# Kernel optimization log

Measured on AMD Instinct MI355X. Metric: run time of the kernel, lower is better.

The kernel has to match this reference:

```python
import jax, jax.numpy as jnp
import numpy as np

C = 1024
H = C // 64          # 16 heads
CH = 64              # head dim
NUM_BUCKETS = 32
MAX_DISTANCE = 64
REL_SCALE = float(np.sqrt(CH))  # (channels//num_heads)**0.5 = 8
EPS = 1e-5


def group_norm(x, gamma, beta, groups):
    # x: [B, C, T]
    B, Cc, T = x.shape
    xg = x.reshape(B, groups, -1)
    m = xg.mean(-1, keepdims=True)
    v = xg.var(-1, keepdims=True)
    xn = ((xg - m) * jax.lax.rsqrt(v + EPS)).reshape(B, Cc, T)
    return xn * gamma[None, :, None] + beta[None, :, None]


def conv1d(x, w, b, pad):
    # x: [B, Cin, T], w: [Cout, Cin, K]
    y = jax.lax.conv_general_dilated(x, w, (1,), [(pad, pad)],
                                     dimension_numbers=('NCH', 'OIH', 'NCH'))
    return y + b[None, :, None]


def rel_pos_bias(T, emb):
    # lucidrains RelativePositionBias, non-causal; emb: [num_buckets, H]
    pos = jnp.arange(T)
    n = pos[:, None] - pos[None, :]          # n = -(k - q) = q - k
    half = NUM_BUCKETS // 2                  # 16
    ret = (n < 0).astype(jnp.int32) * half
    n = jnp.abs(n)
    max_exact = half // 2                    # 8
    is_small = n < max_exact
    nf = jnp.maximum(n, 1).astype(jnp.float32)
    val_large = max_exact + (jnp.log(nf / max_exact)
                             / np.log(MAX_DISTANCE / max_exact)
                             * (half - max_exact)).astype(jnp.int32)
    val_large = jnp.minimum(val_large, half - 1)
    bucket = ret + jnp.where(is_small, n, val_large)  # [T, T]
    return emb[bucket].transpose(2, 0, 1)             # [H, T, T]


def setup_inputs() -> dict:
    key = jax.random.key(0)
    ks = jax.random.split(key, 20)
    B, T = 8, 1024
    s = 0.02
    return {
        'x': jax.random.normal(ks[0], (B, C, T), jnp.float32),
        # ResBlock in_layers
        'rb_gn1_g': jnp.ones((C,), jnp.float32),
        'rb_gn1_b': jnp.zeros((C,), jnp.float32),
        'rb_conv1_w': jax.random.normal(ks[1], (C, C, 3), jnp.float32) * s,
        'rb_conv1_b': jnp.zeros((C,), jnp.float32),
        # ResBlock out_layers (zero-init in original; randomized for testing)
        'rb_gn2_g': jnp.ones((C,), jnp.float32),
        'rb_gn2_b': jnp.zeros((C,), jnp.float32),
        'rb_conv2_w': jax.random.normal(ks[2], (C, C, 3), jnp.float32) * s,
        'rb_conv2_b': jnp.zeros((C,), jnp.float32),
        # outer GroupNorm(8, C)
        'norm_g': jnp.ones((C,), jnp.float32),
        'norm_b': jnp.zeros((C,), jnp.float32),
        # AttentionBlock
        'attn_gn_g': jnp.ones((C,), jnp.float32),
        'attn_gn_b': jnp.zeros((C,), jnp.float32),
        'qkv_w': jax.random.normal(ks[3], (3 * C, C, 1), jnp.float32) * s,
        'qkv_b': jnp.zeros((3 * C,), jnp.float32),
        'proj_w': jax.random.normal(ks[4], (C, C, 1), jnp.float32) * s,
        'proj_b': jnp.zeros((C,), jnp.float32),
        'rel_emb': jax.random.normal(ks[5], (NUM_BUCKETS, H), jnp.float32) * s,
    }


def reference(x, rb_gn1_g, rb_gn1_b, rb_conv1_w, rb_conv1_b,
              rb_gn2_g, rb_gn2_b, rb_conv2_w, rb_conv2_b,
              norm_g, norm_b, attn_gn_g, attn_gn_b,
              qkv_w, qkv_b, proj_w, proj_b, rel_emb):
    B, Cc, T = x.shape
    # ResBlock: GN32 -> SiLU -> conv3 -> GN32 -> SiLU -> (dropout=0) -> conv3, + skip
    h = jax.nn.silu(group_norm(x, rb_gn1_g, rb_gn1_b, 32))
    h = conv1d(h, rb_conv1_w, rb_conv1_b, 1)
    h = jax.nn.silu(group_norm(h, rb_gn2_g, rb_gn2_b, 32))
    h = conv1d(h, rb_conv2_w, rb_conv2_b, 1)
    h = x + h
    # outer GroupNorm(8)
    h = group_norm(h, norm_g, norm_b, 8)
    # AttentionBlock with relative position bias
    xin = h
    qkv = conv1d(group_norm(h, attn_gn_g, attn_gn_b, 32), qkv_w, qkv_b, 0)
    # channel layout after reshape(bs*H, 3*ch, T): [H, 3, ch]
    qkv = qkv.reshape(B, H, 3, CH, T)
    q, k, v = qkv[:, :, 0], qkv[:, :, 1], qkv[:, :, 2]
    scale = CH ** -0.25
    w = jnp.einsum('bhct,bhcs->bhts', q * scale, k * scale)
    bias = rel_pos_bias(T, rel_emb) * REL_SCALE       # [H, T, T]
    w = jax.nn.softmax((w + bias[None]).astype(jnp.float32), axis=-1).astype(w.dtype)
    a = jnp.einsum('bhts,bhcs->bhct', w, v).reshape(B, Cc, T)
    return xin + conv1d(a, proj_w, proj_b, 0)
```

## Files before the change

### kernel.cpp

```cpp
#include <hip/hip_runtime.h>

typedef __attribute__((ext_vector_type(4))) float f32x4;
typedef __attribute__((ext_vector_type(8))) __bf16 bf16x8;
typedef __attribute__((ext_vector_type(4))) unsigned short us4;
typedef __attribute__((ext_vector_type(8))) unsigned short us8;

#define DEVI static __device__ __forceinline__

DEVI unsigned short f2bf(float f){
  union { float f; unsigned u; } x; x.f = f;
  unsigned r = x.u + 0x7fffu + ((x.u >> 16) & 1u);
  return (unsigned short)(r >> 16);
}
DEVI float bf2f(unsigned short h){
  union { unsigned u; float f; } x; x.u = ((unsigned)h) << 16;
  return x.f;
}

typedef __attribute__((address_space(1))) unsigned int gu32;
typedef __attribute__((address_space(3))) unsigned int lu32;
DEVI void gll16(const void* g, void* l){
  __builtin_amdgcn_global_load_lds((gu32*)g, (lu32*)l, 16, 0, 0);
}

DEVI f32x4 mfma16(bf16x8 a, bf16x8 b, f32x4 c){
  return __builtin_amdgcn_mfma_f32_16x16x32_bf16(a, b, c, 0, 0, 0);
}

DEVI float wredsum(float v){
  #pragma unroll
  for (int m = 1; m < 64; m <<= 1) v += __shfl_xor(v, m);
  return v;
}

__global__ __launch_bounds__(256) void conv_w_prep(const float* __restrict__ w,
                                                   unsigned short* __restrict__ wp){
  int idx = blockIdx.x * 256 + threadIdx.x;
  const float* p = w + (size_t)idx * 3;
  wp[idx]           = f2bf(p[0]);
  wp[1048576 + idx] = f2bf(p[1]);
  wp[2097152 + idx] = f2bf(p[2]);
}

__global__ __launch_bounds__(256) void cast_f2b(const float* __restrict__ in,
                                                unsigned short* __restrict__ out, int n4){
  int idx = blockIdx.x * 256 + threadIdx.x;
  if (idx < n4){
    f32x4 v = *(const f32x4*)&in[(size_t)idx * 4];
    us4 o;
    #pragma unroll
    for (int j = 0; j < 4; j++) o[j] = f2bf(v[j]);
    *(us4*)&out[(size_t)idx * 4] = o;
  }
}

__global__ __launch_bounds__(256) void btab_k(const float* __restrict__ emb,
                                              float* __restrict__ btab){
  int idx = blockIdx.x * 256 + threadIdx.x;
  if (idx >= 2047 * 16) return;
  int d = idx >> 4, h = idx & 15;
  int n0 = d - 1023;
  int ret = (n0 < 0) ? 16 : 0;
  int n = (n0 < 0) ? -n0 : n0;
  int bucket;
  if (n < 8) bucket = ret + n;
  else {
    float ratio = logf((float)n * 0.125f) / 2.0794415416798357f;
    int vl = 8 + (int)(ratio * 8.0f);
    bucket = ret + (vl < 15 ? vl : 15);
  }
  btab[h * 2048 + d] = emb[bucket * 16 + h] * 11.541560327111707f;
}

__global__ __launch_bounds__(256) void zero_pads(unsigned short* __restrict__ h1p,
                                                 unsigned short* __restrict__ g2p){
  int idx = blockIdx.x * 256 + threadIdx.x;
  int b = idx >> 11, rr = (idx >> 10) & 1, c = idx & 1023;
  size_t off = ((size_t)b * 1026 + (rr ? 1025 : 0)) * 1024 + c;
  h1p[off] = 0; g2p[off] = 0;
}

__global__ __launch_bounds__(256) void gn_stats_cast(const float* __restrict__ in,
                                                     float2* __restrict__ st,
                                                     unsigned short* __restrict__ xb){
  const int g = blockIdx.x; const int tid = threadIdx.x;
  const float* p = in + (size_t)g * 32768;
  unsigned short* q = xb + (size_t)g * 32768;
  float s = 0.f, s2 = 0.f;
  for (int i = tid * 4; i < 32768; i += 1024){
    f32x4 v = *(const f32x4*)&p[i];
    us4 o;
    #pragma unroll
    for (int j = 0; j < 4; j++){ s += v[j]; s2 += v[j] * v[j]; o[j] = f2bf(v[j]); }
    *(us4*)&q[i] = o;
  }
  s = wredsum(s); s2 = wredsum(s2);
  __shared__ float rs[4], rs2[4];
  if ((tid & 63) == 0){ rs[tid >> 6] = s; rs2[tid >> 6] = s2; }
  __syncthreads();
  if (tid == 0){
    float S = rs[0] + rs[1] + rs[2] + rs[3];
    float S2 = rs2[0] + rs2[1] + rs2[2] + rs2[3];
    float m = S * (1.f / 32768.f);
    float var = S2 * (1.f / 32768.f) - m * m;
    st[g] = make_float2(m, rsqrtf(var + 1e-5f));
  }
}

__global__ __launch_bounds__(256) void gn_stats_bf16(const unsigned short* __restrict__ in,
                                                     float2* __restrict__ st){
  const int g = blockIdx.x; const int tid = threadIdx.x;
  const unsigned short* p = in + (size_t)g * 32768;
  float s = 0.f, s2 = 0.f;
  for (int i = tid * 8; i < 32768; i += 2048){
    us8 v = *(const us8*)&p[i];
    #pragma unroll
    for (int j = 0; j < 8; j++){ float f = bf2f(v[j]); s += f; s2 += f * f; }
  }
  s = wredsum(s); s2 = wredsum(s2);
  __shared__ float rs[4], rs2[4];
  if ((tid & 63) == 0){ rs[tid >> 6] = s; rs2[tid >> 6] = s2; }
  __syncthreads();
  if (tid == 0){
    float S = rs[0] + rs[1] + rs[2] + rs[3];
    float S2 = rs2[0] + rs2[1] + rs2[2] + rs2[3];
    float m = S * (1.f / 32768.f);
    float var = S2 * (1.f / 32768.f) - m * m;
    st[g] = make_float2(m, rsqrtf(var + 1e-5f));
  }
}

template<int SILU, int INBF16, int OUTPAD>
__global__ __launch_bounds__(256) void gn_apply_tr(
    const void* __restrict__ inp, const float2* __restrict__ st,
    const float* __restrict__ gma, const float* __restrict__ bta,
    unsigned short* __restrict__ out)
{
  const int gid = blockIdx.x;
  const int tc = gid & 15, g = (gid >> 4) & 31, b = gid >> 9;
  const int tid = threadIdx.x;
  const int t0 = tc * 64;
  __shared__ __align__(16) unsigned short tr[64 * 40];
  float2 s = st[b * 32 + g];
  int c = tid >> 3, t8 = (tid & 7) * 8;
  int ch = g * 32 + c;
  float sc = gma[ch] * s.y;
  float sh = bta[ch] - s.x * sc;
  float vv[8];
  if (INBF16){
    const unsigned short* p = (const unsigned short*)inp + ((size_t)b * 1024 + ch) * 1024 + t0 + t8;
    us8 v = *(const us8*)p;
    #pragma unroll
    for (int j = 0; j < 8; j++) vv[j] = bf2f(v[j]);
  } else {
    const float* p = (const float*)inp + ((size_t)b * 1024 + ch) * 1024 + t0 + t8;
    f32x4 v0 = *(const f32x4*)p; f32x4 v1 = *(const f32x4*)(p + 4);
    #pragma unroll
    for (int j = 0; j < 4; j++){ vv[j] = v0[j]; vv[4 + j] = v1[j]; }
  }
  #pragma unroll
  for (int j = 0; j < 8; j++){
    float v = vv[j] * sc + sh;
    if (SILU) v = v / (1.f + __expf(-v));
    tr[(t8 + j) * 40 + c] = f2bf(v);
  }
  __syncthreads();
  int t = tid >> 2, c8 = (tid & 3) * 8;
  us8 d = *(const us8*)&tr[t * 40 + c8];
  size_t row = OUTPAD ? ((size_t)b * 1026 + 1 + t0 + t) : ((size_t)b * 1024 + t0 + t);
  *(us8*)&out[row * 1024 + g * 32 + c8] = d;
}

__global__ __launch_bounds__(256) void gn2_partial(const unsigned short* __restrict__ c1,
                                                   float2* __restrict__ part){
  const int tid = threadIdx.x;
  const int ck = blockIdx.x & 31, b = blockIdx.x >> 5;
  const unsigned short* p = c1 + ((size_t)b * 1024 + ck * 32) * 1024 + tid * 4;
  float s = 0.f, s2 = 0.f;
  for (int r = 0; r < 32; r++){
    us4 v = *(const us4*)&p[(size_t)r * 1024];
    #pragma unroll
    for (int j = 0; j < 4; j++){ float f = bf2f(v[j]); s += f; s2 += f * f; }
  }
  __shared__ float ls[256], ls2[256];
  ls[tid] = s; ls2[tid] = s2;
  __syncthreads();
  if (tid < 32){
    float S = 0.f, S2 = 0.f;
    #pragma unroll
    for (int k = 0; k < 8; k++){ S += ls[tid * 8 + k]; S2 += ls2[tid * 8 + k]; }
    part[((size_t)b * 32 + ck) * 32 + tid] = make_float2(S, S2);
  }
}

template<int SILU>
__global__ __launch_bounds__(256) void gn2_apply(const unsigned short* __restrict__ c1,
    const float2* __restrict__ part, const float* __restrict__ gma, const float* __restrict__ bta,
    unsigned short* __restrict__ outp)
{
  const int tid = threadIdx.x;
  const int ck = blockIdx.x & 31, b = blockIdx.x >> 5;
  __shared__ float2 st[32];
  if (tid < 32){
    float S = 0.f, S2 = 0.f;
    for (int k = 0; k < 32; k++){ float2 pp = part[((size_t)b * 32 + k) * 32 + tid]; S += pp.x; S2 += pp.y; }
    float m = S * (1.f / 32768.f);
    float var = S2 * (1.f / 32768.f) - m * m;
    st[tid] = make_float2(m, rsqrtf(var + 1e-5f));
  }
  __syncthreads();
  float2 s = st[tid >> 3];
  float sc[4], sh[4];
  #pragma unroll
  for (int j = 0; j < 4; j++){ int ch = tid * 4 + j; sc[j] = gma[ch] * s.y; sh[j] = bta[ch] - s.x * sc[j]; }
  const unsigned short* p = c1 + ((size_t)b * 1024 + ck * 32) * 1024 + tid * 4;
  unsigned short* q = outp + ((size_t)b * 1026 + 1 + ck * 32) * 1024 + tid * 4;
  for (int r = 0; r < 32; r++){
    us4 v = *(const us4*)&p[(size_t)r * 1024];
    us4 o;
    #pragma unroll
    for (int j = 0; j < 4; j++){
      float f = bf2f(v[j]) * sc[j] + sh[j];
      if (SILU) f = f / (1.f + __expf(-f));
      o[j] = f2bf(f);
    }
    *(us4*)&q[(size_t)r * 1024] = o;
  }
}

__global__ __launch_bounds__(256) void gn8_partial(const unsigned short* __restrict__ r,
                                                   float2* __restrict__ part){
  const int gid = blockIdx.x; const int tid = threadIdx.x;
  const int sub = gid & 15, g = (gid >> 4) & 7, b = gid >> 7;
  const unsigned short* p = r + ((size_t)(b * 8 + g)) * 131072 + sub * 8192;
  float s = 0.f, s2 = 0.f;
  for (int i = tid * 8; i < 8192; i += 2048){
    us8 v = *(const us8*)&p[i];
    #pragma unroll
    for (int j = 0; j < 8; j++){ float f = bf2f(v[j]); s += f; s2 += f * f; }
  }
  s = wredsum(s); s2 = wredsum(s2);
  __shared__ float rs[4], rs2[4];
  if ((tid & 63) == 0){ rs[tid >> 6] = s; rs2[tid >> 6] = s2; }
  __syncthreads();
  if (tid == 0) part[gid] = make_float2(rs[0] + rs[1] + rs[2] + rs[3],
                                        rs2[0] + rs2[1] + rs2[2] + rs2[3]);
}

__global__ __launch_bounds__(256) void gn8_apply(const unsigned short* __restrict__ r,
    const float2* __restrict__ part, const float* __restrict__ gma, const float* __restrict__ bta,
    unsigned short* __restrict__ xin){
  const int gid = blockIdx.x; const int tid = threadIdx.x;
  const int sub = gid & 15, g = (gid >> 4) & 7, b = gid >> 7;
  __shared__ float2 stt;
  if (tid == 0){
    float S = 0.f, S2 = 0.f;
    #pragma unroll
    for (int k = 0; k < 16; k++){ float2 pp = part[(gid & ~15) + k]; S += pp.x; S2 += pp.y; }
    float m = S * (1.f / 131072.f);
    float var = S2 * (1.f / 131072.f) - m * m;
    stt = make_float2(m, rsqrtf(var + 1e-5f));
  }
  __syncthreads();
  float2 s = stt;
  const unsigned short* pr = r + ((size_t)(b * 8 + g)) * 131072 + sub * 8192;
  unsigned short* px = xin + ((size_t)(b * 8 + g)) * 131072 + sub * 8192;
  for (int i = tid * 8; i < 8192; i += 2048){
    int c = g * 128 + sub * 8 + (i >> 10);
    float sc = gma[c] * s.y, sh = bta[c] - s.x * sc;
    us8 v = *(const us8*)&pr[i];
    us8 o;
    #pragma unroll
    for (int j = 0; j < 8; j++) o[j] = f2bf(bf2f(v[j]) * sc + sh);
    *(us8*)&px[i] = o;
  }
}

template<int KK, int EPI>
__global__ __launch_bounds__(256, 2) void gemm_k(
    const unsigned short* __restrict__ inT,
    const unsigned short* __restrict__ W,
    const float* __restrict__ bias,
    void* __restrict__ outp,
    void* __restrict__ resp,
    int OC, int NT)
{
  __shared__ __align__(16) unsigned short Alds[128 * 64];
  __shared__ __align__(16) unsigned short Blds[128 * 64];
  const int tid = threadIdx.x;
  const int lane = tid & 63;
  const int w = tid >> 6;
  const int wn = w >> 1, wo = w & 1;
  const int nt = blockIdx.x % NT;
  const int ot = blockIdx.x / NT;
  const int b = nt >> 3;
  const int t0 = (nt & 7) * 128;
  const int ob = ot * 128;
  const int rowbase = (KK == 3) ? (b * 1026 + t0) : (b * 1024 + t0);

  f32x4 acc[4][4];
  #pragma unroll
  for (int m = 0; m < 4; m++)
    #pragma unroll
    for (int n = 0; n < 4; n++) acc[m][n] = 0.f;

  const int lrow = lane >> 3;
  const int lblk = lane & 7;

  for (int kk = 0; kk < KK; ++kk){
    const unsigned short* Ab = inT + (size_t)(rowbase + kk) * 1024;
    const unsigned short* Bb = W + ((size_t)kk * OC + ob) * 1024;
    for (int i0 = 0; i0 < 1024; i0 += 64){
      #pragma unroll
      for (int j = 0; j < 4; ++j){
        int chunk = w * 4 + j;
        int row = chunk * 8 + lrow;
        int gcol = (lblk ^ (row & 7)) * 8;
        gll16(Ab + (size_t)row * 1024 + i0 + gcol, &Alds[chunk * 512]);
        gll16(Bb + (size_t)row * 1024 + i0 + gcol, &Blds[chunk * 512]);
      }
      __syncthreads();
      bf16x8 af[2][4], bfv[2][4];
      #pragma unroll
      for (int m = 0; m < 4; m++){
        int row = wn * 64 + m * 16 + (lane & 15);
        #pragma unroll
        for (int k2 = 0; k2 < 2; k2++){
          int blk = ((lane >> 4) + k2 * 4) ^ (row & 7);
          af[k2][m] = *(const bf16x8*)&Alds[row * 64 + blk * 8];
        }
      }
      #pragma unroll
      for (int n = 0; n < 4; n++){
        int row = wo * 64 + n * 16 + (lane & 15);
        #pragma unroll
        for (int k2 = 0; k2 < 2; k2++){
          int blk = ((lane >> 4) + k2 * 4) ^ (row & 7);
          bfv[k2][n] = *(const bf16x8*)&Blds[row * 64 + blk * 8];
        }
      }
      #pragma unroll
      for (int k2 = 0; k2 < 2; k2++)
        #pragma unroll
        for (int m = 0; m < 4; m++)
          #pragma unroll
          for (int n = 0; n < 4; n++)
            acc[m][n] = mfma16(af[k2][m], bfv[k2][n], acc[m][n]);
      __syncthreads();
    }
  }

  if (EPI == 0){
    unsigned short* out = (unsigned short*)outp;
    #pragma unroll
    for (int m = 0; m < 4; m++){
      int tl = t0 + wn * 64 + m * 16 + ((lane >> 4) * 4);
      #pragma unroll
      for (int n = 0; n < 4; n++){
        int o = ob + wo * 64 + n * 16 + (lane & 15);
        float bz = bias[o];
        size_t base = ((size_t)b * 1024 + tl) * OC + o;
        #pragma unroll
        for (int r = 0; r < 4; r++)
          out[base + (size_t)r * OC] = f2bf(acc[m][n][r] + bz);
      }
    }
  } else if (EPI == 3){
    unsigned short* qkT = (unsigned short*)outp;
    unsigned short* vT  = (unsigned short*)resp;
    #pragma unroll
    for (int m = 0; m < 4; m++){
      int tl = t0 + wn * 64 + m * 16 + ((lane >> 4) * 4);
      #pragma unroll
      for (int n = 0; n < 4; n++){
        int o0 = ob + wo * 64 + n * 16;
        int h = o0 / 192;
        int rem0 = o0 - h * 192;
        int o = o0 + (lane & 15);
        float bz = bias[o];
        if (rem0 < 128){
          size_t base = ((size_t)b * 1024 + tl) * 2048 + h * 128 + rem0 + (lane & 15);
          #pragma unroll
          for (int r = 0; r < 4; r++)
            qkT[base + (size_t)r * 2048] = f2bf(acc[m][n][r] + bz);
        } else {
          int c = rem0 - 128 + (lane & 15);
          size_t base = (((size_t)(b * 16 + h)) * 64 + c) * 1024 + tl;
          us4 o4;
          #pragma unroll
          for (int r = 0; r < 4; r++) o4[r] = f2bf(acc[m][n][r] + bz);
          *(us4*)&vT[base] = o4;
        }
      }
    }
  } else if (EPI == 4){
    unsigned short* out = (unsigned short*)outp;
    const unsigned short* xr = (const unsigned short*)resp;
    #pragma unroll
    for (int m = 0; m < 4; m++){
      int tl = t0 + wn * 64 + m * 16 + ((lane >> 4) * 4);
      #pragma unroll
      for (int n = 0; n < 4; n++){
        int o = ob + wo * 64 + n * 16 + (lane & 15);
        float bz = bias[o];
        size_t base = ((size_t)b * 1024 + o) * 1024 + tl;
        us4 xv = *(const us4*)&xr[base];
        us4 ov;
        #pragma unroll
        for (int r = 0; r < 4; r++) ov[r] = f2bf(bf2f(xv[r]) + acc[m][n][r] + bz);
        *(us4*)&out[base] = ov;
      }
    }
  } else {
    float* out = (float*)outp;
    #pragma unroll
    for (int m = 0; m < 4; m++){
      int tl = t0 + wn * 64 + m * 16 + ((lane >> 4) * 4);
      #pragma unroll
      for (int n = 0; n < 4; n++){
        int o = ob + wo * 64 + n * 16 + (lane & 15);
        float bz = bias[o];
        size_t base = ((size_t)b * 1024 + o) * 1024 + tl;
        const unsigned short* xr = (const unsigned short*)resp;
        us4 xv = *(const us4*)&xr[base];
        f32x4 v;
        v[0] = bf2f(xv[0]); v[1] = bf2f(xv[1]); v[2] = bf2f(xv[2]); v[3] = bf2f(xv[3]);
        #pragma unroll
        for (int r = 0; r < 4; r++) v[r] += acc[m][n][r] + bz;
        *(f32x4*)&out[base] = v;
      }
    }
  }
}

__global__ __launch_bounds__(256, 2) void attn_k5(
    const unsigned short* __restrict__ qkT,
    const unsigned short* __restrict__ vT,
    const float* __restrict__ btab,
    unsigned short* __restrict__ aT)
{
  __shared__ __align__(16) unsigned short Kb[2][64 * 64];
  __shared__ __align__(16) unsigned short Vb[2][64 * 64];
  __shared__ __align__(16) unsigned short Pb[4][32 * 64];
  __shared__ __align__(16) float blds[1152];
  const int tid = threadIdx.x, lane = tid & 63, w = tid >> 6;
  const int d0 = blockIdx.x;
  const int xcd = d0 & 7, slot = d0 >> 3;
  const int bh = xcd * 16 + (slot >> 3);
  const int qt = slot & 7;
  const int h = bh & 15, b = bh >> 4;
  const int q0b = qt * 128;
  const int q0 = q0b + w * 32;
  const unsigned short* qk = qkT + (size_t)b * 1024 * 2048 + h * 128;
  const unsigned short* vh = vT + ((size_t)(b * 16 + h)) * 64 * 1024;
  const int lc = lane & 15, lg = lane >> 4;

  const float bneg = btab[h * 2048 + 0];
  const float bpos = btab[h * 2048 + 2046];

  for (int i = tid; i < 1151; i += 256)
    blds[i] = btab[h * 2048 + q0b + i];

  bf16x8 qf[2][2];
  #pragma unroll
  for (int m = 0; m < 2; m++){
    const unsigned short* qrow = qk + (size_t)(q0 + m * 16 + lc) * 2048;
    #pragma unroll
    for (int k2 = 0; k2 < 2; k2++)
      qf[m][k2] = *(const bf16x8*)&qrow[k2 * 32 + lg * 8];
  }
  float m_run[2], l_run[2];
  f32x4 oacc[2][4];
  m_run[0] = m_run[1] = -1e30f; l_run[0] = l_run[1] = 0.f;
  #pragma unroll
  for (int m = 0; m < 2; m++)
    #pragma unroll
    for (int cb = 0; cb < 4; cb++) oacc[m][cb] = 0.f;

  const int lr = lane >> 3, lb = lane & 7;
  const float qs = 0.18033688011112042f;

  #pragma unroll
  for (int j = 0; j < 2; j++){
    int chunk = w * 2 + j;
    int row = chunk * 8 + lr;
    int gcol = (lb ^ (row & 7)) * 8;
    gll16(qk + 64 + (size_t)row * 2048 + gcol, &Kb[0][chunk * 512]);
    gll16(vh + (size_t)row * 1024 + gcol, &Vb[0][chunk * 512]);
  }
  __syncthreads();

  for (int t = 0; t < 16; ++t){
    const int cur = t & 1;
    const int st0 = t * 64;
    if (t < 15){
      int nst = st0 + 64;
      #pragma unroll
      for (int j = 0; j < 2; j++){
        int chunk = w * 2 + j;
        int row = chunk * 8 + lr;
        int gcol = (lb ^ (row & 7)) * 8;
        gll16(qk + 64 + (size_t)(nst + row) * 2048 + gcol, &Kb[cur ^ 1][chunk * 512]);
        gll16(vh + (size_t)row * 1024 + nst + gcol, &Vb[cur ^ 1][chunk * 512]);
      }
    }
    f32x4 sfr[2][4];
    #pragma unroll
    for (int m = 0; m < 2; m++)
      #pragma unroll
      for (int sub = 0; sub < 4; sub++) sfr[m][sub] = 0.f;
    __builtin_amdgcn_s_setprio(1);
    #pragma unroll
    for (int sub = 0; sub < 4; sub++){
      int row = sub * 16 + lc;
      #pragma unroll
      for (int k2 = 0; k2 < 2; k2++){
        int blk = (lg + k2 * 4) ^ (row & 7);
        bf16x8 bk = *(const bf16x8*)&Kb[cur][row * 64 + blk * 8];
        sfr[0][sub] = mfma16(bk, qf[0][k2], sfr[0][sub]);
        sfr[1][sub] = mfma16(bk, qf[1][k2], sfr[1][sub]);
      }
    }
    __builtin_amdgcn_s_setprio(0);
    const bool unineg = (st0 >= q0 + 81);
    const bool unipos = (st0 + 113 <= q0);
    const bool uni = unineg || unipos;
    const float bc = unineg ? bneg : bpos;
    float pm2[2];
    if (uni){
      #pragma unroll
      for (int m = 0; m < 2; m++){
        float x0 = fmaxf(fmaxf(sfr[m][0][0], sfr[m][0][1]), fmaxf(sfr[m][0][2], sfr[m][0][3]));
        float x1 = fmaxf(fmaxf(sfr[m][1][0], sfr[m][1][1]), fmaxf(sfr[m][1][2], sfr[m][1][3]));
        float x2 = fmaxf(fmaxf(sfr[m][2][0], sfr[m][2][1]), fmaxf(sfr[m][2][2], sfr[m][2][3]));
        float x3 = fmaxf(fmaxf(sfr[m][3][0], sfr[m][3][1]), fmaxf(sfr[m][3][2], sfr[m][3][3]));
        float pm = fmaxf(fmaxf(x0, x1), fmaxf(x2, x3)) * qs + bc;
        pm = fmaxf(pm, __shfl_xor(pm, 16));
        pm = fmaxf(pm, __shfl_xor(pm, 32));
        pm2[m] = pm;
      }
    } else {
      #pragma unroll
      for (int m = 0; m < 2; m++){
        const float* bp = &blds[(w * 32 + m * 16 + lc) + 960 - st0];
        #pragma unroll
        for (int sub = 0; sub < 4; sub++){
          int off = 63 - sub * 16 - lg * 4;
          #pragma unroll
          for (int r = 0; r < 4; r++)
            sfr[m][sub][r] = sfr[m][sub][r] * qs + bp[off - r];
        }
        float x0 = fmaxf(fmaxf(sfr[m][0][0], sfr[m][0][1]), fmaxf(sfr[m][0][2], sfr[m][0][3]));
        float x1 = fmaxf(fmaxf(sfr[m][1][0], sfr[m][1][1]), fmaxf(sfr[m][1][2], sfr[m][1][3]));
        float x2 = fmaxf(fmaxf(sfr[m][2][0], sfr[m][2][1]), fmaxf(sfr[m][2][2], sfr[m][2][3]));
        float x3 = fmaxf(fmaxf(sfr[m][3][0], sfr[m][3][1]), fmaxf(sfr[m][3][2], sfr[m][3][3]));
        float pm = fmaxf(fmaxf(x0, x1), fmaxf(x2, x3));
        pm = fmaxf(pm, __shfl_xor(pm, 16));
        pm = fmaxf(pm, __shfl_xor(pm, 32));
        pm2[m] = pm;
      }
    }
    const bool stable = (pm2[0] <= m_run[0] + 8.f) && (pm2[1] <= m_run[1] + 8.f);
    const bool resc = !__all(stable);
    float corr[2], mref[2];
    if (resc){
      #pragma unroll
      for (int m = 0; m < 2; m++){
        float mn = fmaxf(m_run[m], pm2[m]);
        corr[m] = exp2f(m_run[m] - mn);
        m_run[m] = mn; mref[m] = mn;
      }
    } else { mref[0] = m_run[0]; mref[1] = m_run[1]; }
    const float scl = uni ? qs : 1.f;
    #pragma unroll
    for (int m = 0; m < 2; m++){
      const float ad = (uni ? bc : 0.f) - mref[m];
      float ssum = 0.f;
      #pragma unroll
      for (int sub = 0; sub < 4; sub++)
        #pragma unroll
        for (int r = 0; r < 4; r++){
          float e = exp2f(fmaf(sfr[m][sub][r], scl, ad));
          sfr[m][sub][r] = e;
          ssum += e;
        }
      ssum += __shfl_xor(ssum, 16);
      ssum += __shfl_xor(ssum, 32);
      l_run[m] = resc ? (l_run[m] * corr[m] + ssum) : (l_run[m] + ssum);
    }
    if (resc){
      #pragma unroll
      for (int m = 0; m < 2; m++)
        #pragma unroll
        for (int r = 0; r < 4; r++){
          float co = __shfl(corr[m], lg * 4 + r);
          #pragma unroll
          for (int cb = 0; cb < 4; cb++) oacc[m][cb][r] *= co;
        }
    }
    unsigned short* P = &Pb[w][0];
    #pragma unroll
    for (int m = 0; m < 2; m++){
      int qrow = m * 16 + lc;
      int rsw = (qrow & 7) << 3;
      #pragma unroll
      for (int sub = 0; sub < 4; sub++){
        int col = sub * 16 + lg * 4;
        unsigned w0, w1;
        asm("v_cvt_pk_bf16_f32 %0, %1, %2" : "=v"(w0) : "v"(sfr[m][sub][0]), "v"(sfr[m][sub][1]));
        asm("v_cvt_pk_bf16_f32 %0, %1, %2" : "=v"(w1) : "v"(sfr[m][sub][2]), "v"(sfr[m][sub][3]));
        uint2 pk; pk.x = w0; pk.y = w1;
        *(uint2*)&P[qrow * 64 + (col ^ rsw)] = pk;
      }
    }
    __builtin_amdgcn_s_setprio(1);
    #pragma unroll
    for (int k2 = 0; k2 < 2; k2++){
      bf16x8 pa[2];
      #pragma unroll
      for (int m = 0; m < 2; m++){
        int rowp = m * 16 + lc;
        int blkp = (lg + k2 * 4) ^ (rowp & 7);
        pa[m] = *(const bf16x8*)&P[rowp * 64 + blkp * 8];
      }
      #pragma unroll
      for (int cb = 0; cb < 4; cb++){
        int ch = cb * 16 + lc;
        int blkv = (lg + k2 * 4) ^ (ch & 7);
        bf16x8 bv = *(const bf16x8*)&Vb[cur][ch * 64 + blkv * 8];
        oacc[0][cb] = mfma16(pa[0], bv, oacc[0][cb]);
        oacc[1][cb] = mfma16(pa[1], bv, oacc[1][cb]);
      }
    }
    __builtin_amdgcn_s_setprio(0);
    __syncthreads();
  }
  #pragma unroll
  for (int m = 0; m < 2; m++)
    #pragma unroll
    for (int r = 0; r < 4; r++){
      float li = 1.0f / __shfl(l_run[m], lg * 4 + r);
      int tq = q0 + m * 16 + lg * 4 + r;
      #pragma unroll
      for (int cb = 0; cb < 4; cb++){
        int ch = h * 64 + cb * 16 + lc;
        aT[((size_t)b * 1024 + tq) * 1024 + ch] = f2bf(oacc[m][cb][r] * li);
      }
    }
}

extern "C" void kernel_launch(void* const* d_in, const int* in_sizes, int n_in,
                              void* d_out, int out_size, void* d_ws, size_t ws_size,
                              hipStream_t stream)
{
  const float* x       = (const float*)d_in[0];
  const float* gn1_g   = (const float*)d_in[1];
  const float* gn1_b   = (const float*)d_in[2];
  const float* conv1_w = (const float*)d_in[3];
  const float* conv1_b = (const float*)d_in[4];
  const float* gn2_g   = (const float*)d_in[5];
  const float* gn2_b   = (const float*)d_in[6];
  const float* conv2_w = (const float*)d_in[7];
  const float* conv2_b = (const float*)d_in[8];
  const float* norm_g  = (const float*)d_in[9];
  const float* norm_b  = (const float*)d_in[10];
  const float* agn_g   = (const float*)d_in[11];
  const float* agn_b   = (const float*)d_in[12];
  const float* qkv_w   = (const float*)d_in[13];
  const float* qkv_b   = (const float*)d_in[14];
  const float* proj_w  = (const float*)d_in[15];
  const float* proj_b  = (const float*)d_in[16];
  const float* rel_emb = (const float*)d_in[17];

  if (ws_size < 139526144u) return;

  char* ws = (char*)d_ws;
  unsigned short* w1p   = (unsigned short*)(ws + 0);
  unsigned short* w2p   = (unsigned short*)(ws + 6291456);
  unsigned short* wqkv  = (unsigned short*)(ws + 12582912);
  unsigned short* wproj = (unsigned short*)(ws + 18874368);
  float* btab           = (float*)(ws + 20971520);
  float2* stats1        = (float2*)(ws + 21102592);
  float2* part2         = (float2*)(ws + 21104640);
  float2* stats32       = (float2*)(ws + 21170176);
  float2* part8         = (float2*)(ws + 21172224);
  unsigned short* h1p   = (unsigned short*)(ws + 22020096);
  unsigned short* c1    = (unsigned short*)(ws + 38830080);
  unsigned short* g2p   = (unsigned short*)(ws + 55607296);
  unsigned short* qkT   = h1p;
  unsigned short* vT    = (unsigned short*)(ws + 55574528);
  unsigned short* xb    = (unsigned short*)(ws + 72417280);
  unsigned short* attn_in = (unsigned short*)(ws + 72417280);
  unsigned short* xin   = (unsigned short*)(ws + 105971712);
  unsigned short* aT    = (unsigned short*)(ws + 122748928);

  conv_w_prep<<<4096, 256, 0, stream>>>(conv1_w, w1p);
  conv_w_prep<<<4096, 256, 0, stream>>>(conv2_w, w2p);
  cast_f2b<<<3072, 256, 0, stream>>>(qkv_w, wqkv, 3072 * 1024 / 4);
  cast_f2b<<<1024, 256, 0, stream>>>(proj_w, wproj, 1024 * 1024 / 4);
  btab_k<<<128, 256, 0, stream>>>(rel_emb, btab);
  zero_pads<<<64, 256, 0, stream>>>(h1p, g2p);

  gn_stats_cast<<<256, 256, 0, stream>>>(x, stats1, xb);
  gn_apply_tr<1, 0, 1><<<4096, 256, 0, stream>>>(x, stats1, gn1_g, gn1_b, h1p);

  gemm_k<3, 0><<<512, 256, 0, stream>>>(h1p, w1p, conv1_b, c1, nullptr, 1024, 64);

  gn2_partial<<<256, 256, 0, stream>>>(c1, part2);
  gn2_apply<1><<<256, 256, 0, stream>>>(c1, part2, gn2_g, gn2_b, g2p);

  gemm_k<3, 4><<<512, 256, 0, stream>>>(g2p, w2p, conv2_b, xb, xb, 1024, 64);

  gn8_partial<<<1024, 256, 0, stream>>>(xb, part8);
  gn8_apply<<<1024, 256, 0, stream>>>(xb, part8, norm_g, norm_b, xin);

  gn_stats_bf16<<<256, 256, 0, stream>>>(xin, stats32);
  gn_apply_tr<0, 1, 0><<<4096, 256, 0, stream>>>(xin, stats32, agn_g, agn_b, attn_in);

  gemm_k<1, 3><<<1536, 256, 0, stream>>>(attn_in, wqkv, qkv_b, qkT, vT, 3072, 64);

  attn_k5<<<1024, 256, 0, stream>>>(qkT, vT, btab, aT);

  gemm_k<1, 2><<<512, 256, 0, stream>>>(aT, wproj, proj_b, d_out, xin, 1024, 64);
}
```

Measured before the change: 381.0 us.

## Double-buffer GEMM LDS tiles with async prefetch; store attention bias table as bf16

The GEMM main loop is restructured into a two-stage software pipeline. Global-to-LDS loads for tile k+2 are issued right after the fragment reads from the current buffer, using explicit vmcnt waits, barriers and raised priority around the MFMA block. This is meant to hide global load latency that the previous load-sync-compute-sync loop exposed. LDS use per block doubles to 64KB, which may limit occupancy. Separately, the attention kernel keeps its relative-bias table in LDS as bf16 instead of fp32, which shrinks LDS but rounds the bias values.

```diff
diff --git a/kernel.cpp b/kernel.cpp
--- a/kernel.cpp
+++ b/kernel.cpp
@@ -285,8 +285,8 @@
     void* __restrict__ resp,
     int OC, int NT)
 {
-  __shared__ __align__(16) unsigned short Alds[128 * 64];
-  __shared__ __align__(16) unsigned short Blds[128 * 64];
+  __shared__ __align__(16) unsigned short Alds[2][128 * 64];
+  __shared__ __align__(16) unsigned short Blds[2][128 * 64];
   const int tid = threadIdx.x;
   const int lane = tid & 63;
   const int w = tid >> 6;
@@ -297,6 +297,7 @@
   const int t0 = (nt & 7) * 128;
   const int ob = ot * 128;
   const int rowbase = (KK == 3) ? (b * 1026 + t0) : (b * 1024 + t0);
+  const int NTI = KK * 16;
 
   f32x4 acc[4][4];
   #pragma unroll
@@ -307,47 +308,73 @@
   const int lrow = lane >> 3;
   const int lblk = lane & 7;
 
-  for (int kk = 0; kk < KK; ++kk){
+  auto stage = [&](int kt, int bufsel){
+    int kk = kt >> 4;
+    int i0 = (kt & 15) * 64;
     const unsigned short* Ab = inT + (size_t)(rowbase + kk) * 1024;
     const unsigned short* Bb = W + ((size_t)kk * OC + ob) * 1024;
-    for (int i0 = 0; i0 < 1024; i0 += 64){
-      #pragma unroll
-      for (int j = 0; j < 4; ++j){
-        int chunk = w * 4 + j;
-        int row = chunk * 8 + lrow;
-        int gcol = (lblk ^ (row & 7)) * 8;
-        gll16(Ab + (size_t)row * 1024 + i0 + gcol, &Alds[chunk * 512]);
-        gll16(Bb + (size_t)row * 1024 + i0 + gcol, &Blds[chunk * 512]);
-      }
-      __syncthreads();
-      bf16x8 af[2][4], bfv[2][4];
-      #pragma unroll
-      for (int m = 0; m < 4; m++){
-        int row = wn * 64 + m * 16 + (lane & 15);
+    #pragma unroll
+    for (int j = 0; j < 4; ++j){
+      int chunk = w * 4 + j;
+      int row = chunk * 8 + lrow;
+      int gcol = (lblk ^ (row & 7)) * 8;
+      gll16(Ab + (size_t)row * 1024 + i0 + gcol, &Alds[bufsel][chunk * 512]);
+      gll16(Bb + (size_t)row * 1024 + i0 + gcol, &Blds[bufsel][chunk * 512]);
+    }
+  };
+
+  stage(0, 0);
+  stage(1, 1);
+  asm volatile("s_waitcnt vmcnt(8)" ::: "memory");
+  __builtin_amdgcn_sched_barrier(0);
+  __builtin_amdgcn_s_barrier();
+  __builtin_amdgcn_sched_barrier(0);
+
+  #pragma unroll 2
+  for (int kt = 0; kt < NTI; ++kt){
+    const int cur = kt & 1;
+    const unsigned short* Ab = &Alds[cur][0];
+    const unsigned short* Bb = &Blds[cur][0];
+    bf16x8 af[2][4], bfv[2][4];
+    #pragma unroll
+    for (int m = 0; m < 4; m++){
+      int row = wn * 64 + m * 16 + (lane & 15);
+      #pragma unroll
+      for (int k2 = 0; k2 < 2; k2++){
+        int blk = ((lane >> 4) + k2 * 4) ^ (row & 7);
+        af[k2][m] = *(const bf16x8*)&Ab[row * 64 + blk * 8];
+      }
+    }
+    #pragma unroll
+    for (int n = 0; n < 4; n++){
+      int row = wo * 64 + n * 16 + (lane & 15);
+      #pragma unroll
+      for (int k2 = 0; k2 < 2; k2++){
+        int blk = ((lane >> 4) + k2 * 4) ^ (row & 7);
+        bfv[k2][n] = *(const bf16x8*)&Bb[row * 64 + blk * 8];
+      }
+    }
+    asm volatile("s_waitcnt lgkmcnt(0)" ::: "memory");
+    __builtin_amdgcn_sched_barrier(0);
+    __builtin_amdgcn_s_barrier();
+    __builtin_amdgcn_sched_barrier(0);
+    if (kt + 2 < NTI) stage(kt + 2, cur);
+    __builtin_amdgcn_sched_barrier(0);
+    __builtin_amdgcn_s_setprio(1);
+    #pragma unroll
+    for (int k2 = 0; k2 < 2; k2++)
+      #pragma unroll
+      for (int m = 0; m < 4; m++)
         #pragma unroll
-        for (int k2 = 0; k2 < 2; k2++){
-          int blk = ((lane >> 4) + k2 * 4) ^ (row & 7);
-          af[k2][m] = *(const bf16x8*)&Alds[row * 64 + blk * 8];
-        }
-      }
-      #pragma unroll
-      for (int n = 0; n < 4; n++){
-        int row = wo * 64 + n * 16 + (lane & 15);
-        #pragma unroll
-        for (int k2 = 0; k2 < 2; k2++){
-          int blk = ((lane >> 4) + k2 * 4) ^ (row & 7);
-          bfv[k2][n] = *(const bf16x8*)&Blds[row * 64 + blk * 8];
-        }
-      }
-      #pragma unroll
-      for (int k2 = 0; k2 < 2; k2++)
-        #pragma unroll
-        for (int m = 0; m < 4; m++)
-          #pragma unroll
-          for (int n = 0; n < 4; n++)
-            acc[m][n] = mfma16(af[k2][m], bfv[k2][n], acc[m][n]);
-      __syncthreads();
-    }
+        for (int n = 0; n < 4; n++)
+          acc[m][n] = mfma16(af[k2][m], bfv[k2][n], acc[m][n]);
+    __builtin_amdgcn_s_setprio(0);
+    __builtin_amdgcn_sched_barrier(0);
+    if (kt + 2 < NTI){ asm volatile("s_waitcnt vmcnt(8)" ::: "memory"); }
+    else             { asm volatile("s_waitcnt vmcnt(0)" ::: "memory"); }
+    __builtin_amdgcn_sched_barrier(0);
+    __builtin_amdgcn_s_barrier();
+    __builtin_amdgcn_sched_barrier(0);
   }
 
   if (EPI == 0){
@@ -433,7 +460,7 @@
   }
 }
 
-__global__ __launch_bounds__(256, 2) void attn_k5(
+__global__ __launch_bounds__(256, 2) void attn_k6(
     const unsigned short* __restrict__ qkT,
     const unsigned short* __restrict__ vT,
     const float* __restrict__ btab,
@@ -442,7 +469,7 @@
   __shared__ __align__(16) unsigned short Kb[2][64 * 64];
   __shared__ __align__(16) unsigned short Vb[2][64 * 64];
   __shared__ __align__(16) unsigned short Pb[4][32 * 64];
-  __shared__ __align__(16) float blds[1152];
+  __shared__ __align__(16) unsigned short blds[1152];
   const int tid = threadIdx.x, lane = tid & 63, w = tid >> 6;
   const int d0 = blockIdx.x;
   const int xcd = d0 & 7, slot = d0 >> 3;
@@ -459,7 +486,7 @@
   const float bpos = btab[h * 2048 + 2046];
 
   for (int i = tid; i < 1151; i += 256)
-    blds[i] = btab[h * 2048 + q0b + i];
+    blds[i] = f2bf(btab[h * 2048 + q0b + i]);
 
   bf16x8 qf[2][2];
   #pragma unroll
@@ -542,13 +569,13 @@
     } else {
       #pragma unroll
       for (int m = 0; m < 2; m++){
-        const float* bp = &blds[(w * 32 + m * 16 + lc) + 960 - st0];
+        const unsigned short* bp = &blds[(w * 32 + m * 16 + lc) + 960 - st0];
         #pragma unroll
         for (int sub = 0; sub < 4; sub++){
           int off = 63 - sub * 16 - lg * 4;
           #pragma unroll
           for (int r = 0; r < 4; r++)
-            sfr[m][sub][r] = sfr[m][sub][r] * qs + bp[off - r];
+            sfr[m][sub][r] = sfr[m][sub][r] * qs + bf2f(bp[off - r]);
         }
         float x0 = fmaxf(fmaxf(sfr[m][0][0], sfr[m][0][1]), fmaxf(sfr[m][0][2], sfr[m][0][3]));
         float x1 = fmaxf(fmaxf(sfr[m][1][0], sfr[m][1][1]), fmaxf(sfr[m][1][2], sfr[m][1][3]));
@@ -719,7 +746,7 @@
 
   gemm_k<1, 3><<<1536, 256, 0, stream>>>(attn_in, wqkv, qkv_b, qkT, vT, 3072, 64);
 
-  attn_k5<<<1024, 256, 0, stream>>>(qkT, vT, btab, aT);
+  attn_k6<<<1024, 256, 0, stream>>>(qkT, vT, btab, aT);
 
   gemm_k<1, 2><<<512, 256, 0, stream>>>(aT, wproj, proj_b, d_out, xin, 1024, 64);
 }
```

New measurement: 372.6 us. -2.2%, faster.
